# Optimization experiments

Hardware: AMD Instinct MI355X
Metric: run time of the kernel (lower is better)

The kernel has to match this reference:

```python
import jax, jax.numpy as jnp
import numpy as np

D_IN = 768
D_OUT = 768
NUM_HEADS = 12
HEAD_DIM = D_OUT // NUM_HEADS


def setup_inputs() -> dict:
    key = jax.random.key(0)
    ks = jax.random.split(key, 6)
    s = 0.02
    x = jax.random.normal(ks[0], (4, 1024, D_IN), dtype=jnp.float32)
    # torch Linear weights are [out_features, in_features]
    Wq = jax.random.normal(ks[1], (D_OUT, D_IN), dtype=jnp.float32) * s
    Wk = jax.random.normal(ks[2], (D_OUT, D_IN), dtype=jnp.float32) * s
    Wv = jax.random.normal(ks[3], (D_OUT, D_IN), dtype=jnp.float32) * s
    Wo = jax.random.normal(ks[4], (D_OUT, D_OUT), dtype=jnp.float32) * s
    bo = jax.random.normal(ks[5], (D_OUT,), dtype=jnp.float32) * s
    return {"x": x, "Wq": Wq, "Wk": Wk, "Wv": Wv, "Wo": Wo, "bo": bo}


def reference(x, Wq, Wk, Wv, Wo, bo):
    B, T, _ = x.shape
    H, Dh = NUM_HEADS, HEAD_DIM
    # QKV projections (no bias), reshape to [B, H, T, Dh]
    q = (x @ Wq.T).reshape(B, T, H, Dh).transpose(0, 2, 1, 3)
    k = (x @ Wk.T).reshape(B, T, H, Dh).transpose(0, 2, 1, 3)
    v = (x @ Wv.T).reshape(B, T, H, Dh).transpose(0, 2, 1, 3)
    # Scores [B, H, T, T]. NOTE: original torch code's masked_fill and dropout
    # are not in-place / not assigned, so neither affects the output.
    scores = jnp.einsum("bhqd,bhkd->bhqk", q, k)
    attn = jax.nn.softmax(scores / np.sqrt(Dh).astype(np.float32), axis=-1)
    ctx = jnp.einsum("bhqk,bhkd->bhqd", attn, v)
    ctx = ctx.transpose(0, 2, 1, 3).reshape(B, T, H * Dh)
    return ctx @ Wo.T + bo
```

## Files before the change

### kernel.cpp

```cpp
#include <hip/hip_runtime.h>

typedef _Float16 half8 __attribute__((ext_vector_type(8)));
typedef float f32x4 __attribute__((ext_vector_type(4)));
typedef unsigned short u16;

#define NHEAD 12
#define DHEAD 64
#define DM    768
#define TSEQ  1024
#define LOG2E 1.44269504f

static constexpr size_t OFF_XH  = 0;
static constexpr size_t OFF_WQH = 3145728;
static constexpr size_t OFF_WKH = 3735552;
static constexpr size_t OFF_WVH = 4325376;
static constexpr size_t OFF_WOH = 4915200;
static constexpr size_t OFF_Q   = 5505024;
static constexpr size_t OFF_K   = 8650752;
static constexpr size_t OFF_VT  = 11796480;
static constexpr size_t OFF_CTX = 0;
static constexpr size_t OFF_OP  = 14942208;
static constexpr size_t OFF_ML_BYTES = 42467328;
static constexpr size_t WS_NEED_SPLITK = 43253760;

typedef const __attribute__((address_space(1))) void* gas_ptr;
typedef __attribute__((address_space(3))) void* las_ptr;
__device__ __forceinline__ void gload16(const _Float16* g, _Float16* l) {
    __builtin_amdgcn_global_load_lds((gas_ptr)g, (las_ptr)l, 16, 0, 0);
}

template <int CTRL>
__device__ __forceinline__ float dpp_rotf(float x) {
    int r = __builtin_amdgcn_update_dpp(0, __builtin_bit_cast(int, x), CTRL, 0xF, 0xF, true);
    return __builtin_bit_cast(float, r);
}
__device__ __forceinline__ float row16_max(float x) {
    x = fmaxf(x, dpp_rotf<0x121>(x));
    x = fmaxf(x, dpp_rotf<0x122>(x));
    x = fmaxf(x, dpp_rotf<0x124>(x));
    x = fmaxf(x, dpp_rotf<0x128>(x));
    return x;
}
__device__ __forceinline__ float row16_add(float x) {
    x = x + dpp_rotf<0x121>(x);
    x = x + dpp_rotf<0x122>(x);
    x = x + dpp_rotf<0x124>(x);
    x = x + dpp_rotf<0x128>(x);
    return x;
}

__global__ void cvt_kernel(const float* __restrict__ x, const float* __restrict__ wq,
                           const float* __restrict__ wk, const float* __restrict__ wv,
                           const float* __restrict__ wo, _Float16* __restrict__ ws) {
    int seg = blockIdx.y;
    const float* src;
    _Float16* dst;
    int n;
    if (seg == 0)      { src = x;  dst = ws + OFF_XH;  n = 3145728; }
    else if (seg == 1) { src = wq; dst = ws + OFF_WQH; n = 589824; }
    else if (seg == 2) { src = wk; dst = ws + OFF_WKH; n = 589824; }
    else if (seg == 3) { src = wv; dst = ws + OFF_WVH; n = 589824; }
    else               { src = wo; dst = ws + OFF_WOH; n = 589824; }
    int i = (blockIdx.x * blockDim.x + threadIdx.x) * 8;
    if (i < n) {
        float4 v0 = *(const float4*)(src + i);
        float4 v1 = *(const float4*)(src + i + 4);
        half8 o;
        o[0] = (_Float16)v0.x; o[1] = (_Float16)v0.y;
        o[2] = (_Float16)v0.z; o[3] = (_Float16)v0.w;
        o[4] = (_Float16)v1.x; o[5] = (_Float16)v1.y;
        o[6] = (_Float16)v1.z; o[7] = (_Float16)v1.w;
        *(half8*)(dst + i) = o;
    }
}

__global__ __launch_bounds__(256) void qkv_kernel(_Float16* __restrict__ ws) {
    __shared__ __align__(16) _Float16 ldsA[128 * 32];
    __shared__ __align__(16) _Float16 ldsB[128 * 32];

    const int z = blockIdx.z;
    const _Float16* __restrict__ xh = ws + OFF_XH;
    const _Float16* __restrict__ w  = ws + (z == 0 ? OFF_WQH : z == 1 ? OFF_WKH : OFF_WVH);
    _Float16* __restrict__ outp     = ws + (z == 0 ? OFF_Q   : z == 1 ? OFF_K   : OFF_VT);

    const int tid  = threadIdx.x;
    const int lane = tid & 63;
    const int wid  = tid >> 6;
    const int quad = lane >> 4, l15 = lane & 15;
    const int wm = (wid & 1) * 64, wn = (wid >> 1) * 64;

    int mb, nb;
    const _Float16 *gA, *gB;
    if (z < 2) {
        mb = blockIdx.x * 128;
        nb = blockIdx.y * 128;
        gA = xh + (size_t)mb * DM;
        gB = w  + (size_t)nb * DM;
    } else {
        mb = blockIdx.y * 128;
        nb = blockIdx.x * 128;
        gA = w  + (size_t)mb * DM;
        gB = xh + (size_t)nb * DM;
    }

    const int srow = (lane >> 2);
    const int scol = (lane & 3) * 8;
    const size_t goff0 = (size_t)(wid * 32 + srow) * DM + scol;
    const size_t goff1 = (size_t)(wid * 32 + 16 + srow) * DM + scol;
    _Float16* lA0 = ldsA + wid * 1024;
    _Float16* lA1 = ldsA + wid * 1024 + 512;
    _Float16* lB0 = ldsB + wid * 1024;
    _Float16* lB1 = ldsB + wid * 1024 + 512;

    f32x4 acc[4][4] = {};
    for (int k0 = 0; k0 < DM; k0 += 32) {
        gload16(gA + goff0 + k0, lA0);
        gload16(gA + goff1 + k0, lA1);
        gload16(gB + goff0 + k0, lB0);
        gload16(gB + goff1 + k0, lB1);
        __syncthreads();

        half8 a[4], b[4];
#pragma unroll
        for (int t = 0; t < 4; t++) {
            a[t] = *(const half8*)(ldsA + (wm + t * 16 + l15) * 32 + quad * 8);
            b[t] = *(const half8*)(ldsB + (wn + t * 16 + l15) * 32 + quad * 8);
        }
#pragma unroll
        for (int mt = 0; mt < 4; mt++)
#pragma unroll
            for (int nt = 0; nt < 4; nt++)
                acc[mt][nt] = __builtin_amdgcn_mfma_f32_16x16x32_f16(a[mt], b[nt], acc[mt][nt], 0, 0, 0);
        __syncthreads();
    }

#pragma unroll
    for (int mt = 0; mt < 4; mt++)
#pragma unroll
        for (int nt = 0; nt < 4; nt++)
#pragma unroll
            for (int r = 0; r < 4; r++) {
                int m = mb + wm + mt * 16 + quad * 4 + r;
                int n = nb + wn + nt * 16 + l15;
                size_t idx;
                if (z < 2) {
                    int bb = m >> 10, tt = m & 1023;
                    int h = n >> 6, d = n & 63;
                    idx = ((size_t)(bb * NHEAD + h) * TSEQ + tt) * DHEAD + d;
                } else {
                    int h = m >> 6, d = m & 63;
                    int bb = n >> 10, tt = n & 1023;
                    idx = ((size_t)(bb * NHEAD + h) * DHEAD + d) * TSEQ + tt;
                }
                outp[idx] = (_Float16)acc[mt][nt][r];
            }
}

template <int NZ>
__device__ __forceinline__ void attn_body(_Float16* __restrict__ ws) {
    __shared__ __align__(16) _Float16 ldsK[64 * 64];
    __shared__ __align__(16) _Float16 ldsV[64 * 64];
    __shared__ __align__(16) _Float16 ldsP[4][16 * 72];

    const int tid  = threadIdx.x;
    const int lane = tid & 63;
    const int wid  = tid >> 6;
    const int quad = lane >> 4, l15 = lane & 15;
    const int bh = blockIdx.y;
    const int z  = (NZ > 1) ? blockIdx.z : 0;
    const int q0 = blockIdx.x * 64 + wid * 16;
    const int kbeg = z * (TSEQ / NZ), kend = kbeg + TSEQ / NZ;

    const _Float16* __restrict__ Q  = ws + OFF_Q  + (size_t)bh * TSEQ * DHEAD;
    const _Float16* __restrict__ K  = ws + OFF_K  + (size_t)bh * TSEQ * DHEAD;
    const _Float16* __restrict__ VT = ws + OFF_VT + (size_t)bh * DHEAD * TSEQ;
    _Float16* pbase = ldsP[wid];

    const int srow0 = tid >> 3, sc0 = tid & 7;
    const int ldsOff0 = srow0 * 64 + ((sc0 ^ (srow0 & 7)) * 8);
    const int ldsOff1 = (srow0 + 32) * 64 + ((sc0 ^ (srow0 & 7)) * 8);

    half8 qf[2];
#pragma unroll
    for (int ks = 0; ks < 2; ks++) {
        qf[ks] = *(const half8*)(Q + (size_t)(q0 + l15) * DHEAD + ks * 32 + quad * 8);
        qf[ks] = qf[ks] * (_Float16)0.125f;
    }

    float mrun[4], lrun[4];
    f32x4 oacc[4] = {};
#pragma unroll
    for (int r = 0; r < 4; r++) { mrun[r] = -1e30f; lrun[r] = 0.f; }

    uint4 ka, kb, va, vb;
    ka = *(const uint4*)(K + kbeg * DHEAD + tid * 8);
    kb = *(const uint4*)(K + kbeg * DHEAD + 2048 + tid * 8);
    va = *(const uint4*)(VT + (size_t)srow0 * TSEQ + kbeg + sc0 * 8);
    vb = *(const uint4*)(VT + (size_t)(srow0 + 32) * TSEQ + kbeg + sc0 * 8);

    for (int kt = kbeg; kt < kend; kt += 64) {
        *(uint4*)(ldsK + ldsOff0) = ka;
        *(uint4*)(ldsK + ldsOff1) = kb;
        *(uint4*)(ldsV + ldsOff0) = va;
        *(uint4*)(ldsV + ldsOff1) = vb;
        __syncthreads();

        if (kt + 64 < kend) {
            ka = *(const uint4*)(K + (kt + 64) * DHEAD + tid * 8);
            kb = *(const uint4*)(K + (kt + 64) * DHEAD + 2048 + tid * 8);
            va = *(const uint4*)(VT + (size_t)srow0 * TSEQ + kt + 64 + sc0 * 8);
            vb = *(const uint4*)(VT + (size_t)(srow0 + 32) * TSEQ + kt + 64 + sc0 * 8);
        }

        half8 kf[4][2];
#pragma unroll
        for (int n = 0; n < 4; n++)
#pragma unroll
            for (int ks = 0; ks < 2; ks++) {
                int row = n * 16 + l15;
                int phys = (ks * 4 + quad) ^ (row & 7);
                kf[n][ks] = *(const half8*)(ldsK + row * 64 + phys * 8);
            }

        f32x4 s[4] = {};
#pragma unroll
        for (int n = 0; n < 4; n++)
#pragma unroll
            for (int ks = 0; ks < 2; ks++)
                s[n] = __builtin_amdgcn_mfma_f32_16x16x32_f16(qf[ks], kf[n][ks], s[n], 0, 0, 0);

#pragma unroll
        for (int r = 0; r < 4; r++) {
            float tm = fmaxf(fmaxf(s[0][r], s[1][r]), fmaxf(s[2][r], s[3][r]));
            tm = row16_max(tm);
            float mnew = fmaxf(mrun[r], tm);
            float alpha = __builtin_amdgcn_exp2f((mrun[r] - mnew) * LOG2E);
            mrun[r] = mnew;
            float mL = mnew * LOG2E;
            float ts = 0.f;
#pragma unroll
            for (int n = 0; n < 4; n++) {
                float e = __builtin_amdgcn_exp2f(__builtin_fmaf(s[n][r], LOG2E, -mL));
                s[n][r] = e;
                ts += e;
            }
            ts = row16_add(ts);
            lrun[r] = __builtin_fmaf(lrun[r], alpha, ts);
#pragma unroll
            for (int dn = 0; dn < 4; dn++) oacc[dn][r] *= alpha;
        }

#pragma unroll
        for (int n = 0; n < 4; n++)
#pragma unroll
            for (int r = 0; r < 4; r++)
                pbase[(quad * 4 + r) * 72 + n * 16 + l15] = (_Float16)s[n][r];

        half8 vf[4][2];
#pragma unroll
        for (int dn = 0; dn < 4; dn++)
#pragma unroll
            for (int ks = 0; ks < 2; ks++) {
                int row = dn * 16 + l15;
                int phys = (ks * 4 + quad) ^ (row & 7);
                vf[dn][ks] = *(const half8*)(ldsV + row * 64 + phys * 8);
            }

        half8 pf[2];
#pragma unroll
        for (int ks = 0; ks < 2; ks++)
            pf[ks] = *(const half8*)(pbase + l15 * 72 + ks * 32 + quad * 8);

#pragma unroll
        for (int dn = 0; dn < 4; dn++)
#pragma unroll
            for (int ks = 0; ks < 2; ks++)
                oacc[dn] = __builtin_amdgcn_mfma_f32_16x16x32_f16(pf[ks], vf[dn][ks], oacc[dn], 0, 0, 0);

        __syncthreads();
    }

    if (NZ == 1) {
        _Float16* __restrict__ ctx = ws + OFF_CTX;
        const int b_ = bh / NHEAD, h = bh % NHEAD;
#pragma unroll
        for (int dn = 0; dn < 4; dn++)
#pragma unroll
            for (int r = 0; r < 4; r++) {
                int t_ = q0 + quad * 4 + r;
                int col = h * DHEAD + dn * 16 + l15;
                float v = oacc[dn][r] / lrun[r];
                ctx[((size_t)(b_ * TSEQ + t_)) * DM + col] = (_Float16)v;
            }
    } else {
        _Float16* __restrict__ op = ws + OFF_OP;
        float* __restrict__ ml = (float*)((char*)ws + OFF_ML_BYTES);
        const size_t rowbase = (size_t)z * 48 * TSEQ + (size_t)bh * TSEQ + q0;
#pragma unroll
        for (int dn = 0; dn < 4; dn++)
#pragma unroll
            for (int r = 0; r < 4; r++) {
                size_t row = rowbase + quad * 4 + r;
                op[row * 64 + dn * 16 + l15] = (_Float16)oacc[dn][r];
            }
        if (l15 == 0) {
#pragma unroll
            for (int r = 0; r < 4; r++) {
                size_t row = rowbase + quad * 4 + r;
                ml[row * 2]     = mrun[r];
                ml[row * 2 + 1] = lrun[r];
            }
        }
    }
}

__global__ __launch_bounds__(256, 3) void attn_kernel(_Float16* __restrict__ ws) {
    attn_body<1>(ws);
}
__global__ __launch_bounds__(256, 4) void attn_splitk_kernel(_Float16* __restrict__ ws) {
    attn_body<2>(ws);
}

__global__ __launch_bounds__(256) void combine_kernel(_Float16* __restrict__ ws) {
    const _Float16* __restrict__ op = ws + OFF_OP;
    const float* __restrict__ ml = (const float*)((const char*)ws + OFF_ML_BYTES);
    _Float16* __restrict__ ctx = ws + OFF_CTX;

    int g = blockIdx.x * 256 + threadIdx.x;
    int row = g >> 3, chunk = g & 7;
    int bh = row >> 10, q = row & 1023;
    int b_ = bh / NHEAD, h = bh % NHEAD;

    float m0 = ml[(size_t)row * 2], l0 = ml[(size_t)row * 2 + 1];
    float m1 = ml[(size_t)(49152 + row) * 2], l1 = ml[(size_t)(49152 + row) * 2 + 1];
    float M = fmaxf(m0, m1);
    float w0 = __builtin_amdgcn_exp2f((m0 - M) * LOG2E);
    float w1 = __builtin_amdgcn_exp2f((m1 - M) * LOG2E);
    float inv_l = 1.0f / (w0 * l0 + w1 * l1);

    half8 o0 = *(const half8*)(op + (size_t)row * 64 + chunk * 8);
    half8 o1 = *(const half8*)(op + (size_t)(49152 + row) * 64 + chunk * 8);
    half8 o;
#pragma unroll
    for (int j = 0; j < 8; j++)
        o[j] = (_Float16)(((float)o0[j] * w0 + (float)o1[j] * w1) * inv_l);
    *(half8*)(ctx + ((size_t)(b_ * TSEQ + q)) * DM + h * DHEAD + chunk * 8) = o;
}

__global__ __launch_bounds__(256) void proj_kernel(const _Float16* __restrict__ ws,
                                                   const float* __restrict__ bo,
                                                   float* __restrict__ out) {
    __shared__ __align__(16) _Float16 ldsA[64 * 32];
    __shared__ __align__(16) _Float16 ldsB[64 * 32];

    const _Float16* __restrict__ gA = ws + OFF_CTX + (size_t)blockIdx.x * 64 * DM;
    const _Float16* __restrict__ gB = ws + OFF_WOH + (size_t)blockIdx.y * 64 * DM;

    const int tid  = threadIdx.x;
    const int lane = tid & 63;
    const int wid  = tid >> 6;
    const int quad = lane >> 4, l15 = lane & 15;
    const int wm = (wid & 1) * 32, wn = (wid >> 1) * 32;

    const int srow = tid >> 2;
    const int scol = (tid & 3) * 8;
    const size_t goff = (size_t)srow * DM + scol;
    _Float16* lA = ldsA + wid * 512;
    _Float16* lB = ldsB + wid * 512;

    f32x4 acc[2][2] = {};
    for (int k0 = 0; k0 < DM; k0 += 32) {
        gload16(gA + goff + k0, lA);
        gload16(gB + goff + k0, lB);
        __syncthreads();

        half8 a[2], b[2];
#pragma unroll
        for (int t = 0; t < 2; t++) {
            a[t] = *(const half8*)(ldsA + (wm + t * 16 + l15) * 32 + quad * 8);
            b[t] = *(const half8*)(ldsB + (wn + t * 16 + l15) * 32 + quad * 8);
        }
#pragma unroll
        for (int mt = 0; mt < 2; mt++)
#pragma unroll
            for (int nt = 0; nt < 2; nt++)
                acc[mt][nt] = __builtin_amdgcn_mfma_f32_16x16x32_f16(a[mt], b[nt], acc[mt][nt], 0, 0, 0);
        __syncthreads();
    }

    const int mb = blockIdx.x * 64, nb = blockIdx.y * 64;
#pragma unroll
    for (int mt = 0; mt < 2; mt++)
#pragma unroll
        for (int nt = 0; nt < 2; nt++)
#pragma unroll
            for (int r = 0; r < 4; r++) {
                int m = mb + wm + mt * 16 + quad * 4 + r;
                int n = nb + wn + nt * 16 + l15;
                out[(size_t)m * DM + n] = acc[mt][nt][r] + bo[n];
            }
}

extern "C" void kernel_launch(void* const* d_in, const int* in_sizes, int n_in,
                              void* d_out, int out_size, void* d_ws, size_t ws_size,
                              hipStream_t stream) {
    const float* x  = (const float*)d_in[0];
    const float* wq = (const float*)d_in[1];
    const float* wk = (const float*)d_in[2];
    const float* wv = (const float*)d_in[3];
    const float* wo = (const float*)d_in[4];
    const float* bo = (const float*)d_in[5];
    _Float16* ws = (_Float16*)d_ws;
    float* out = (float*)d_out;

    cvt_kernel<<<dim3(1536, 5, 1), 256, 0, stream>>>(x, wq, wk, wv, wo, ws);
    qkv_kernel<<<dim3(32, 6, 3), 256, 0, stream>>>(ws);
    if (ws_size >= WS_NEED_SPLITK) {
        attn_splitk_kernel<<<dim3(16, 48, 2), 256, 0, stream>>>(ws);
        combine_kernel<<<dim3(1536, 1, 1), 256, 0, stream>>>(ws);
    } else {
        attn_kernel<<<dim3(16, 48, 1), 256, 0, stream>>>(ws);
    }
    proj_kernel<<<dim3(64, 12, 1), 256, 0, stream>>>(ws, bo, out);
}
```

Measured before the change: 147.8 us.

## Process two 16-row query tiles per wave in attention to reuse K/V fragments

Each wave now handles 32 query rows (two 16-row MFMA tiles) instead of 16, so every K and V fragment read from LDS feeds two MFMAs. The block covers 128 queries and the grid x-dimension is halved. The P staging buffer grows and its row stride changes to 76 to alter the LDS bank pattern. The cost is higher register pressure (the split-k launch bound drops to 3 waves) and half as many blocks, which reduces parallelism on a large-CU GPU.

```diff
diff --git a/kernel.cpp b/kernel.cpp
--- a/kernel.cpp
+++ b/kernel.cpp
@@ -156,11 +156,12 @@
             }
 }
 
+#define PSTR 76
 template <int NZ>
 __device__ __forceinline__ void attn_body(_Float16* __restrict__ ws) {
     __shared__ __align__(16) _Float16 ldsK[64 * 64];
     __shared__ __align__(16) _Float16 ldsV[64 * 64];
-    __shared__ __align__(16) _Float16 ldsP[4][16 * 72];
+    __shared__ __align__(16) _Float16 ldsP[4][32 * PSTR];
 
     const int tid  = threadIdx.x;
     const int lane = tid & 63;
@@ -168,7 +169,7 @@
     const int quad = lane >> 4, l15 = lane & 15;
     const int bh = blockIdx.y;
     const int z  = (NZ > 1) ? blockIdx.z : 0;
-    const int q0 = blockIdx.x * 64 + wid * 16;
+    const int q0 = blockIdx.x * 128 + wid * 32;
     const int kbeg = z * (TSEQ / NZ), kend = kbeg + TSEQ / NZ;
 
     const _Float16* __restrict__ Q  = ws + OFF_Q  + (size_t)bh * TSEQ * DHEAD;
@@ -180,17 +181,21 @@
     const int ldsOff0 = srow0 * 64 + ((sc0 ^ (srow0 & 7)) * 8);
     const int ldsOff1 = (srow0 + 32) * 64 + ((sc0 ^ (srow0 & 7)) * 8);
 
-    half8 qf[2];
-#pragma unroll
-    for (int ks = 0; ks < 2; ks++) {
-        qf[ks] = *(const half8*)(Q + (size_t)(q0 + l15) * DHEAD + ks * 32 + quad * 8);
-        qf[ks] = qf[ks] * (_Float16)0.125f;
-    }
-
-    float mrun[4], lrun[4];
-    f32x4 oacc[4] = {};
-#pragma unroll
-    for (int r = 0; r < 4; r++) { mrun[r] = -1e30f; lrun[r] = 0.f; }
+    half8 qf[2][2];
+#pragma unroll
+    for (int mt = 0; mt < 2; mt++)
+#pragma unroll
+        for (int ks = 0; ks < 2; ks++) {
+            qf[mt][ks] = *(const half8*)(Q + (size_t)(q0 + mt * 16 + l15) * DHEAD + ks * 32 + quad * 8);
+            qf[mt][ks] = qf[mt][ks] * (_Float16)0.125f;
+        }
+
+    float mrun[2][4], lrun[2][4];
+    f32x4 oacc[2][4] = {};
+#pragma unroll
+    for (int mt = 0; mt < 2; mt++)
+#pragma unroll
+        for (int r = 0; r < 4; r++) { mrun[mt][r] = -1e30f; lrun[mt][r] = 0.f; }
 
     uint4 ka, kb, va, vb;
     ka = *(const uint4*)(K + kbeg * DHEAD + tid * 8);
@@ -212,70 +217,66 @@
             vb = *(const uint4*)(VT + (size_t)(srow0 + 32) * TSEQ + kt + 64 + sc0 * 8);
         }
 
-        half8 kf[4][2];
-#pragma unroll
-        for (int n = 0; n < 4; n++)
-#pragma unroll
-            for (int ks = 0; ks < 2; ks++) {
-                int row = n * 16 + l15;
-                int phys = (ks * 4 + quad) ^ (row & 7);
-                kf[n][ks] = *(const half8*)(ldsK + row * 64 + phys * 8);
+        f32x4 s[2][4] = {};
+#pragma unroll
+        for (int n = 0; n < 4; n++) {
+            int row = n * 16 + l15;
+            half8 kf0 = *(const half8*)(ldsK + row * 64 + ((0 * 4 + quad) ^ (row & 7)) * 8);
+            half8 kf1 = *(const half8*)(ldsK + row * 64 + ((1 * 4 + quad) ^ (row & 7)) * 8);
+            s[0][n] = __builtin_amdgcn_mfma_f32_16x16x32_f16(qf[0][0], kf0, s[0][n], 0, 0, 0);
+            s[1][n] = __builtin_amdgcn_mfma_f32_16x16x32_f16(qf[1][0], kf0, s[1][n], 0, 0, 0);
+            s[0][n] = __builtin_amdgcn_mfma_f32_16x16x32_f16(qf[0][1], kf1, s[0][n], 0, 0, 0);
+            s[1][n] = __builtin_amdgcn_mfma_f32_16x16x32_f16(qf[1][1], kf1, s[1][n], 0, 0, 0);
+        }
+
+#pragma unroll
+        for (int mt = 0; mt < 2; mt++)
+#pragma unroll
+            for (int r = 0; r < 4; r++) {
+                float tm = fmaxf(fmaxf(s[mt][0][r], s[mt][1][r]), fmaxf(s[mt][2][r], s[mt][3][r]));
+                tm = row16_max(tm);
+                float mnew = fmaxf(mrun[mt][r], tm);
+                float alpha = __builtin_amdgcn_exp2f((mrun[mt][r] - mnew) * LOG2E);
+                mrun[mt][r] = mnew;
+                float mL = mnew * LOG2E;
+                float ts = 0.f;
+#pragma unroll
+                for (int n = 0; n < 4; n++) {
+                    float e = __builtin_amdgcn_exp2f(__builtin_fmaf(s[mt][n][r], LOG2E, -mL));
+                    s[mt][n][r] = e;
+                    ts += e;
+                }
+                ts = row16_add(ts);
+                lrun[mt][r] = __builtin_fmaf(lrun[mt][r], alpha, ts);
+#pragma unroll
+                for (int dn = 0; dn < 4; dn++) oacc[mt][dn][r] *= alpha;
             }
 
-        f32x4 s[4] = {};
-#pragma unroll
-        for (int n = 0; n < 4; n++)
+#pragma unroll
+        for (int mt = 0; mt < 2; mt++)
+#pragma unroll
+            for (int n = 0; n < 4; n++)
+#pragma unroll
+                for (int r = 0; r < 4; r++)
+                    pbase[(mt * 16 + quad * 4 + r) * PSTR + n * 16 + l15] = (_Float16)s[mt][n][r];
+
+        half8 pf[2][2];
+#pragma unroll
+        for (int mt = 0; mt < 2; mt++)
 #pragma unroll
             for (int ks = 0; ks < 2; ks++)
-                s[n] = __builtin_amdgcn_mfma_f32_16x16x32_f16(qf[ks], kf[n][ks], s[n], 0, 0, 0);
-
-#pragma unroll
-        for (int r = 0; r < 4; r++) {
-            float tm = fmaxf(fmaxf(s[0][r], s[1][r]), fmaxf(s[2][r], s[3][r]));
-            tm = row16_max(tm);
-            float mnew = fmaxf(mrun[r], tm);
-            float alpha = __builtin_amdgcn_exp2f((mrun[r] - mnew) * LOG2E);
-            mrun[r] = mnew;
-            float mL = mnew * LOG2E;
-            float ts = 0.f;
-#pragma unroll
-            for (int n = 0; n < 4; n++) {
-                float e = __builtin_amdgcn_exp2f(__builtin_fmaf(s[n][r], LOG2E, -mL));
-                s[n][r] = e;
-                ts += e;
-            }
-            ts = row16_add(ts);
-            lrun[r] = __builtin_fmaf(lrun[r], alpha, ts);
-#pragma unroll
-            for (int dn = 0; dn < 4; dn++) oacc[dn][r] *= alpha;
-        }
-
-#pragma unroll
-        for (int n = 0; n < 4; n++)
-#pragma unroll
-            for (int r = 0; r < 4; r++)
-                pbase[(quad * 4 + r) * 72 + n * 16 + l15] = (_Float16)s[n][r];
-
-        half8 vf[4][2];
-#pragma unroll
-        for (int dn = 0; dn < 4; dn++)
-#pragma unroll
-            for (int ks = 0; ks < 2; ks++) {
-                int row = dn * 16 + l15;
-                int phys = (ks * 4 + quad) ^ (row & 7);
-                vf[dn][ks] = *(const half8*)(ldsV + row * 64 + phys * 8);
-            }
-
-        half8 pf[2];
-#pragma unroll
-        for (int ks = 0; ks < 2; ks++)
-            pf[ks] = *(const half8*)(pbase + l15 * 72 + ks * 32 + quad * 8);
-
-#pragma unroll
-        for (int dn = 0; dn < 4; dn++)
-#pragma unroll
-            for (int ks = 0; ks < 2; ks++)
-                oacc[dn] = __builtin_amdgcn_mfma_f32_16x16x32_f16(pf[ks], vf[dn][ks], oacc[dn], 0, 0, 0);
+                pf[mt][ks] = *(const half8*)(pbase + (mt * 16 + l15) * PSTR + ks * 32 + quad * 8);
+
+#pragma unroll
+        for (int dn = 0; dn < 4; dn++) {
+            int row = dn * 16 + l15;
+            half8 vf0 = *(const half8*)(ldsV + row * 64 + ((0 * 4 + quad) ^ (row & 7)) * 8);
+            half8 vf1 = *(const half8*)(ldsV + row * 64 + ((1 * 4 + quad) ^ (row & 7)) * 8);
+            oacc[0][dn] = __builtin_amdgcn_mfma_f32_16x16x32_f16(pf[0][0], vf0, oacc[0][dn], 0, 0, 0);
+            oacc[1][dn] = __builtin_amdgcn_mfma_f32_16x16x32_f16(pf[1][0], vf0, oacc[1][dn], 0, 0, 0);
+            oacc[0][dn] = __builtin_amdgcn_mfma_f32_16x16x32_f16(pf[0][1], vf1, oacc[0][dn], 0, 0, 0);
+            oacc[1][dn] = __builtin_amdgcn_mfma_f32_16x16x32_f16(pf[1][1], vf1, oacc[1][dn], 0, 0, 0);
+        }
 
         __syncthreads();
     }
@@ -284,32 +285,38 @@
         _Float16* __restrict__ ctx = ws + OFF_CTX;
         const int b_ = bh / NHEAD, h = bh % NHEAD;
 #pragma unroll
-        for (int dn = 0; dn < 4; dn++)
-#pragma unroll
-            for (int r = 0; r < 4; r++) {
-                int t_ = q0 + quad * 4 + r;
-                int col = h * DHEAD + dn * 16 + l15;
-                float v = oacc[dn][r] / lrun[r];
-                ctx[((size_t)(b_ * TSEQ + t_)) * DM + col] = (_Float16)v;
-            }
+        for (int mt = 0; mt < 2; mt++)
+#pragma unroll
+            for (int dn = 0; dn < 4; dn++)
+#pragma unroll
+                for (int r = 0; r < 4; r++) {
+                    int t_ = q0 + mt * 16 + quad * 4 + r;
+                    int col = h * DHEAD + dn * 16 + l15;
+                    float v = oacc[mt][dn][r] / lrun[mt][r];
+                    ctx[((size_t)(b_ * TSEQ + t_)) * DM + col] = (_Float16)v;
+                }
     } else {
         _Float16* __restrict__ op = ws + OFF_OP;
         float* __restrict__ ml = (float*)((char*)ws + OFF_ML_BYTES);
         const size_t rowbase = (size_t)z * 48 * TSEQ + (size_t)bh * TSEQ + q0;
 #pragma unroll
-        for (int dn = 0; dn < 4; dn++)
-#pragma unroll
-            for (int r = 0; r < 4; r++) {
-                size_t row = rowbase + quad * 4 + r;
-                op[row * 64 + dn * 16 + l15] = (_Float16)oacc[dn][r];
-            }
+        for (int mt = 0; mt < 2; mt++)
+#pragma unroll
+            for (int dn = 0; dn < 4; dn++)
+#pragma unroll
+                for (int r = 0; r < 4; r++) {
+                    size_t row = rowbase + mt * 16 + quad * 4 + r;
+                    op[row * 64 + dn * 16 + l15] = (_Float16)oacc[mt][dn][r];
+                }
         if (l15 == 0) {
 #pragma unroll
-            for (int r = 0; r < 4; r++) {
-                size_t row = rowbase + quad * 4 + r;
-                ml[row * 2]     = mrun[r];
-                ml[row * 2 + 1] = lrun[r];
-            }
+            for (int mt = 0; mt < 2; mt++)
+#pragma unroll
+                for (int r = 0; r < 4; r++) {
+                    size_t row = rowbase + mt * 16 + quad * 4 + r;
+                    ml[row * 2]     = mrun[mt][r];
+                    ml[row * 2 + 1] = lrun[mt][r];
+                }
         }
     }
 }
@@ -317,7 +324,7 @@
 __global__ __launch_bounds__(256, 3) void attn_kernel(_Float16* __restrict__ ws) {
     attn_body<1>(ws);
 }
-__global__ __launch_bounds__(256, 4) void attn_splitk_kernel(_Float16* __restrict__ ws) {
+__global__ __launch_bounds__(256, 3) void attn_splitk_kernel(_Float16* __restrict__ ws) {
     attn_body<2>(ws);
 }
 
@@ -416,10 +423,10 @@
     cvt_kernel<<<dim3(1536, 5, 1), 256, 0, stream>>>(x, wq, wk, wv, wo, ws);
     qkv_kernel<<<dim3(32, 6, 3), 256, 0, stream>>>(ws);
     if (ws_size >= WS_NEED_SPLITK) {
-        attn_splitk_kernel<<<dim3(16, 48, 2), 256, 0, stream>>>(ws);
+        attn_splitk_kernel<<<dim3(8, 48, 2), 256, 0, stream>>>(ws);
         combine_kernel<<<dim3(1536, 1, 1), 256, 0, stream>>>(ws);
     } else {
-        attn_kernel<<<dim3(16, 48, 1), 256, 0, stream>>>(ws);
+        attn_kernel<<<dim3(8, 48, 1), 256, 0, stream>>>(ws);
     }
     proj_kernel<<<dim3(64, 12, 1), 256, 0, stream>>>(ws, bo, out);
 }
```

New measurement: 155.4 us. 5.1% more time.
